# Optimization experiments

Measured on AMD Instinct MI355X. Metric: run time of the kernel, lower is better.

## Reference

```python
import jax, jax.numpy as jnp
import numpy as np

EMBED_DIM = 1024
NUM_HEADS = 16
HEAD_DIM = EMBED_DIM // NUM_HEADS
SCALE = HEAD_DIM ** -0.5
B, T = 4, 2048


def setup_inputs() -> dict:
    key = jax.random.key(0)
    ks = jax.random.split(key, 5)
    s = EMBED_DIM ** -0.5
    return {
        "x": jax.random.normal(ks[0], (B, T, EMBED_DIM), dtype=jnp.float32),
        "w_qkv": jax.random.normal(ks[1], (EMBED_DIM, 3 * EMBED_DIM), dtype=jnp.float32) * s,
        "b_qkv": jnp.zeros((3 * EMBED_DIM,), dtype=jnp.float32),
        "w_out": jax.random.normal(ks[2], (EMBED_DIM, EMBED_DIM), dtype=jnp.float32) * s,
        "b_out": jnp.zeros((EMBED_DIM,), dtype=jnp.float32),
    }


def reference(x, w_qkv, b_qkv, w_out, b_out):
    Bz, Tz, C = x.shape
    qkv = x @ w_qkv + b_qkv                              # (B,T,3C)
    qkv = qkv.reshape(Bz, Tz, 3, NUM_HEADS, HEAD_DIM)
    q, k, v = (qkv[:, :, i].transpose(0, 2, 1, 3) for i in range(3))  # (B,H,T,Dh)
    attn = jnp.einsum('bhqd,bhkd->bhqk', q, k) * SCALE   # (B,H,T,T)
    attn = jax.nn.softmax(attn, axis=-1)
    out = jnp.einsum('bhqk,bhkd->bhqd', attn, v)         # (B,H,T,Dh)
    out = out.transpose(0, 2, 1, 3).reshape(Bz, Tz, C)
    return out @ w_out + b_out
```

## Files before the change

kernel.cpp:

```cpp
#include <hip/hip_runtime.h>
#include <stdint.h>

#define EMB   1024
#define NH    16
#define DH    64
#define NB    4
#define NT    2048
#define BT    (NB*NT)
#define NQKV  (3*EMB)
#define CL2E  0.1803368801111204f

typedef short v4s __attribute__((ext_vector_type(4)));
typedef short v8s __attribute__((ext_vector_type(8)));
typedef float v4f __attribute__((ext_vector_type(4)));

__device__ __forceinline__ unsigned short f2bf(float f) {
  unsigned int u = __builtin_bit_cast(unsigned int, f);
  u += 0x7fffu + ((u >> 16) & 1u);
  return (unsigned short)(u >> 16);
}

__device__ __forceinline__ void gld16(const unsigned short* g, unsigned short* l) {
  __builtin_amdgcn_global_load_lds(
      (const __attribute__((address_space(1))) unsigned int*)g,
      (__attribute__((address_space(3))) unsigned int*)l, 16, 0, 0);
}

__device__ __forceinline__ v4s exppack(v4f s) {
  unsigned int u0 = __builtin_bit_cast(unsigned int, exp2f(s[0])) + 0x8000u;
  unsigned int u1 = __builtin_bit_cast(unsigned int, exp2f(s[1])) + 0x8000u;
  unsigned int u2 = __builtin_bit_cast(unsigned int, exp2f(s[2])) + 0x8000u;
  unsigned int u3 = __builtin_bit_cast(unsigned int, exp2f(s[3])) + 0x8000u;
  uint2 d;
  d.x = __builtin_amdgcn_perm(u1, u0, 0x07060302u);
  d.y = __builtin_amdgcn_perm(u3, u2, 0x07060302u);
  return __builtin_bit_cast(v4s, d);
}

__global__ __launch_bounds__(256) void cast_bf16_k(
    const float* __restrict__ in, unsigned short* __restrict__ out, int n8) {
  int i = blockIdx.x * 256 + threadIdx.x;
  if (i >= n8) return;
  const float4* p = (const float4*)in + (size_t)i * 2;
  float4 a = p[0], b = p[1];
  union { unsigned short s[8]; uint4 u; } o;
  o.s[0] = f2bf(a.x); o.s[1] = f2bf(a.y); o.s[2] = f2bf(a.z); o.s[3] = f2bf(a.w);
  o.s[4] = f2bf(b.x); o.s[5] = f2bf(b.y); o.s[6] = f2bf(b.z); o.s[7] = f2bf(b.w);
  ((uint4*)out)[i] = o.u;
}

__global__ __launch_bounds__(256) void transpose_cast_k(
    const float* __restrict__ in, unsigned short* __restrict__ out, int R, int C) {
  __shared__ float tile[32][33];
  int t = threadIdx.x, lr = t >> 5, lc = t & 31;
  int r0 = blockIdx.y * 32, c0 = blockIdx.x * 32;
#pragma unroll
  for (int i = 0; i < 32; i += 8)
    tile[lr + i][lc] = in[(size_t)(r0 + lr + i) * C + c0 + lc];
  __syncthreads();
#pragma unroll
  for (int i = 0; i < 32; i += 8)
    out[(size_t)(c0 + lr + i) * R + r0 + lc] = f2bf(tile[lc][lr + i]);
}

template <int MODE>
__global__ __launch_bounds__(256, 2) void gemm_bt(
    const unsigned short* __restrict__ A, const unsigned short* __restrict__ Bt,
    const float* __restrict__ bias, float* __restrict__ Co,
    unsigned short* __restrict__ q_out, unsigned short* __restrict__ k_out,
    unsigned short* __restrict__ v_out, int M, int N, int K) {
  const int t = threadIdx.x;
  const int wave = t >> 6, lane = t & 63;
  const int m16 = lane & 15, quad = lane >> 4;
  const int wr = wave >> 1, wc = wave & 1;
  const int bm = blockIdx.y * 128, bn = blockIdx.x * 128;

  __shared__ unsigned short As[128 * 32];
  __shared__ unsigned short Bs[128 * 32];

  v4f acc[4][4];
#pragma unroll
  for (int mi = 0; mi < 4; mi++)
#pragma unroll
    for (int ni = 0; ni < 4; ni++) acc[mi][ni] = (v4f){0.f, 0.f, 0.f, 0.f};

  const int sF = (m16 ^ (m16 >> 2)) & 3;

  const int cA = t, rA = cA >> 2, jA = (cA & 3) ^ ((rA ^ (rA >> 2)) & 3);
  const int cB = 256 + t, rB = cB >> 2, jB = (cB & 3) ^ ((rB ^ (rB >> 2)) & 3);
  const unsigned short* gA0 = A + (size_t)(bm + rA) * K + jA * 8;
  const unsigned short* gA1 = A + (size_t)(bm + rB) * K + jB * 8;
  const unsigned short* gB0 = Bt + (size_t)(bn + rA) * K + jA * 8;
  const unsigned short* gB1 = Bt + (size_t)(bn + rB) * K + jB * 8;
  const unsigned short* aBase = &As[(wr * 64 + m16) * 32 + ((quad ^ sF) * 8)];
  const unsigned short* bBase = &Bs[(wc * 64 + m16) * 32 + ((quad ^ sF) * 8)];

  const int nkt = K >> 5;
  for (int kt = 0; kt < nkt; ++kt) {
    gld16(gA0, &As[cA * 8]);
    gld16(gA1, &As[cB * 8]);
    gld16(gB0, &Bs[cA * 8]);
    gld16(gB1, &Bs[cB * 8]);
    gA0 += 32; gA1 += 32; gB0 += 32; gB1 += 32;
    __syncthreads();

    v8s a[4], b[4];
#pragma unroll
    for (int mi = 0; mi < 4; mi++)
      a[mi] = *(const v8s*)(aBase + mi * 16 * 32);
#pragma unroll
    for (int ni = 0; ni < 4; ni++)
      b[ni] = *(const v8s*)(bBase + ni * 16 * 32);
#pragma unroll
    for (int mi = 0; mi < 4; mi++)
#pragma unroll
      for (int ni = 0; ni < 4; ni++)
        acc[mi][ni] = __builtin_amdgcn_mfma_f32_16x16x32_bf16(a[mi], b[ni], acc[mi][ni], 0, 0, 0);
    __syncthreads();
  }

  if (MODE == 0) {
#pragma unroll
    for (int mi = 0; mi < 4; mi++) {
#pragma unroll
      for (int ni = 0; ni < 4; ni++) {
        int col = bn + wc * 64 + ni * 16 + m16;
        int which = col >> 10;
        int h = (col >> 6) & 15, d = col & 63;
        float bv = bias[col];
        float sc = (which == 0) ? CL2E : 1.f;
        int row0 = bm + wr * 64 + mi * 16 + quad * 4;
        int bb = row0 >> 11, tt0 = row0 & 2047;
        float v0 = (acc[mi][ni][0] + bv) * sc, v1 = (acc[mi][ni][1] + bv) * sc;
        float v2 = (acc[mi][ni][2] + bv) * sc, v3 = (acc[mi][ni][3] + bv) * sc;
        if (which == 2) {
          ushort4 pk; pk.x = f2bf(v0); pk.y = f2bf(v1); pk.z = f2bf(v2); pk.w = f2bf(v3);
          *(ushort4*)&v_out[(((size_t)(bb * NH + h)) * DH + d) * NT + tt0] = pk;
        } else {
          unsigned short* dst = (which == 0) ? q_out : k_out;
          size_t idx = (((size_t)(bb * NH + h)) * NT + tt0) * DH + d;
          dst[idx] = f2bf(v0); dst[idx + DH] = f2bf(v1);
          dst[idx + 2 * DH] = f2bf(v2); dst[idx + 3 * DH] = f2bf(v3);
        }
      }
    }
  } else {
#pragma unroll
    for (int mi = 0; mi < 4; mi++) {
#pragma unroll
      for (int ni = 0; ni < 4; ni++) {
        int col = bn + wc * 64 + ni * 16 + m16;
        float bv = bias[col];
#pragma unroll
        for (int r = 0; r < 4; r++) {
          int row = bm + wr * 64 + mi * 16 + quad * 4 + r;
          Co[(size_t)row * N + col] = acc[mi][ni][r] + bv;
        }
      }
    }
  }
}

__global__ __launch_bounds__(256, 3) void flash_attn(
    const unsigned short* __restrict__ Qg, const unsigned short* __restrict__ Kg,
    const unsigned short* __restrict__ Vtg, unsigned short* __restrict__ Og) {
  const int t = threadIdx.x;
  const int w = t >> 6, lane = t & 63;
  const int m16 = lane & 15, quad = lane >> 4;
  const int qt = blockIdx.x, bh = blockIdx.y;
  const int b = bh >> 4, h = bh & 15;

  __shared__ unsigned short Ks[128 * 64];
  __shared__ unsigned short Vt[64 * 128];

  const size_t baseq = (size_t)bh * NT * DH;
  const size_t basev = (size_t)bh * DH * NT;

  v8s qf[2][2];
#pragma unroll
  for (int tq = 0; tq < 2; tq++) {
    int qrow = qt * 128 + w * 32 + tq * 16 + m16;
#pragma unroll
    for (int kk = 0; kk < 2; kk++)
      qf[tq][kk] = *(const v8s*)&Qg[baseq + (size_t)qrow * DH + kk * 32 + quad * 8];
  }

  v4f accO[2][4], accL[2];
#pragma unroll
  for (int tq = 0; tq < 2; tq++) {
#pragma unroll
    for (int i = 0; i < 4; i++) accO[tq][i] = (v4f){0.f, 0.f, 0.f, 0.f};
    accL[tq] = (v4f){0.f, 0.f, 0.f, 0.f};
  }
  const v4f zero4 = (v4f){0.f, 0.f, 0.f, 0.f};
  const v4s ones4 = (v4s){(short)0x3F80, (short)0x3F80, (short)0x3F80, (short)0x3F80};

  const int sK = m16 & 7;
  const int rK = t >> 3, jK = (t & 7) ^ (rK & 7);
  const int dV = t >> 4, jV = (t & 15) ^ (dV & 15);
  const unsigned short* gK = &Kg[baseq + (size_t)rK * DH + jK * 8];
  const unsigned short* gV = &Vtg[basev + (size_t)dV * NT + jV * 8];
  const unsigned short* kb0 = &Ks[m16 * 64 + (((0 * 4 + quad) ^ sK) * 8)];
  const unsigned short* kb1 = &Ks[m16 * 64 + (((1 * 4 + quad) ^ sK) * 8)];
  const int qh = quad >> 1, q1 = quad & 1;
  const unsigned short* vBase = &Vt[m16 * 128 + q1 * 4];

  for (int kt = 0; kt < NT / 128; ++kt) {
    __syncthreads();
#pragma unroll
    for (int i = 0; i < 4; ++i)
      gld16(gK + (size_t)(i * 32) * DH, &Ks[(i * 256 + t) * 8]);
#pragma unroll
    for (int i = 0; i < 4; ++i)
      gld16(gV + (size_t)(i * 16) * NT, &Vt[(i * 256 + t) * 8]);
    gK += 128 * DH;
    gV += 128;
    __syncthreads();

    v4s pp[2][8];
#pragma unroll
    for (int ni = 0; ni < 8; ni++) {
      v8s k0 = *(const v8s*)(kb0 + ni * 1024);
      v8s k1 = *(const v8s*)(kb1 + ni * 1024);
      v4f s0 = __builtin_amdgcn_mfma_f32_16x16x32_bf16(k0, qf[0][0], zero4, 0, 0, 0);
      s0 = __builtin_amdgcn_mfma_f32_16x16x32_bf16(k1, qf[0][1], s0, 0, 0, 0);
      v4f s1 = __builtin_amdgcn_mfma_f32_16x16x32_bf16(k0, qf[1][0], zero4, 0, 0, 0);
      s1 = __builtin_amdgcn_mfma_f32_16x16x32_bf16(k1, qf[1][1], s1, 0, 0, 0);
      pp[0][ni] = exppack(s0);
      pp[1][ni] = exppack(s1);
    }

#pragma unroll
    for (int ni = 0; ni < 8; ni++) {
      accL[0] = __builtin_amdgcn_mfma_f32_16x16x16bf16_1k(ones4, pp[0][ni], accL[0], 0, 0, 0);
      accL[1] = __builtin_amdgcn_mfma_f32_16x16x16bf16_1k(ones4, pp[1][ni], accL[1], 0, 0, 0);
      const unsigned short* vA = vBase + (((ni * 2 + qh) ^ m16) * 8);
#pragma unroll
      for (int ni2 = 0; ni2 < 4; ni2++) {
        v4s vf = *(const v4s*)(vA + ni2 * 2048);
        accO[0][ni2] = __builtin_amdgcn_mfma_f32_16x16x16bf16_1k(vf, pp[0][ni], accO[0][ni2], 0, 0, 0);
        accO[1][ni2] = __builtin_amdgcn_mfma_f32_16x16x16bf16_1k(vf, pp[1][ni], accO[1][ni2], 0, 0, 0);
      }
    }
  }

#pragma unroll
  for (int tq = 0; tq < 2; tq++) {
    float inv = 1.f / accL[tq][0];
    int trow = qt * 128 + w * 32 + tq * 16 + m16;
    size_t ob = ((size_t)b * NT + trow) * EMB + h * DH;
#pragma unroll
    for (int ni2 = 0; ni2 < 4; ni2++) {
      float v0 = accO[tq][ni2][0] * inv, v1 = accO[tq][ni2][1] * inv;
      float v2 = accO[tq][ni2][2] * inv, v3 = accO[tq][ni2][3] * inv;
      uint2 d;
      d.x = (unsigned int)f2bf(v0) | ((unsigned int)f2bf(v1) << 16);
      d.y = (unsigned int)f2bf(v2) | ((unsigned int)f2bf(v3) << 16);
      *(uint2*)&Og[ob + ni2 * 16 + quad * 4] = d;
    }
  }
}

extern "C" void kernel_launch(void* const* d_in, const int* in_sizes, int n_in,
                              void* d_out, int out_size, void* d_ws, size_t ws_size,
                              hipStream_t stream) {
  const float* x     = (const float*)d_in[0];
  const float* w_qkv = (const float*)d_in[1];
  const float* b_qkv = (const float*)d_in[2];
  const float* w_out = (const float*)d_in[3];
  const float* b_out = (const float*)d_in[4];
  float* out = (float*)d_out;

  unsigned short* xb    = (unsigned short*)d_ws;
  unsigned short* wqkvT = xb    + (size_t)BT * EMB;
  unsigned short* woutT = wqkvT + (size_t)NQKV * EMB;
  unsigned short* qb    = woutT + (size_t)EMB * EMB;
  unsigned short* kb    = qb    + (size_t)NB * NH * NT * DH;
  unsigned short* vb    = kb    + (size_t)NB * NH * NT * DH;
  unsigned short* ao    = vb    + (size_t)NB * NH * NT * DH;

  cast_bf16_k<<<(BT * EMB / 8 + 255) / 256, 256, 0, stream>>>(x, xb, BT * EMB / 8);
  transpose_cast_k<<<dim3(NQKV / 32, EMB / 32), 256, 0, stream>>>(w_qkv, wqkvT, EMB, NQKV);
  transpose_cast_k<<<dim3(EMB / 32, EMB / 32), 256, 0, stream>>>(w_out, woutT, EMB, EMB);

  gemm_bt<0><<<dim3(NQKV / 128, BT / 128), 256, 0, stream>>>(
      xb, wqkvT, b_qkv, nullptr, qb, kb, vb, BT, NQKV, EMB);

  flash_attn<<<dim3(NT / 128, NB * NH), 256, 0, stream>>>(qb, kb, vb, ao);

  gemm_bt<1><<<dim3(EMB / 128, BT / 128), 256, 0, stream>>>(
      ao, woutT, b_out, out, nullptr, nullptr, nullptr, BT, EMB, EMB);
}
```

Before: 310.0 us.

## Use 16x16x32 bf16 MFMA for PV with remapped K layout and packed exp conversion

The PV and row-sum products switch from 16x16x16 MFMAs to 16x16x32 MFMAs, which halves the instruction count. To supply that, the K tile in LDS gets a new swizzle and key mapping so each lane's two QK^T results form the 8 contiguous keys the wider B operand needs. Exponentials now use the native exp2 builtin and the hardware v_cvt_pk_bf16_f32 instruction in place of manual rounding bit tricks. The risks are LDS bank conflicts from the new swizzle and a subtle key-order mismatch between the P fragments and the V reads.

```diff
diff --git a/kernel.cpp b/kernel.cpp
--- a/kernel.cpp
+++ b/kernel.cpp
@@ -26,15 +26,19 @@
       (__attribute__((address_space(3))) unsigned int*)l, 16, 0, 0);
 }
 
-__device__ __forceinline__ v4s exppack(v4f s) {
-  unsigned int u0 = __builtin_bit_cast(unsigned int, exp2f(s[0])) + 0x8000u;
-  unsigned int u1 = __builtin_bit_cast(unsigned int, exp2f(s[1])) + 0x8000u;
-  unsigned int u2 = __builtin_bit_cast(unsigned int, exp2f(s[2])) + 0x8000u;
-  unsigned int u3 = __builtin_bit_cast(unsigned int, exp2f(s[3])) + 0x8000u;
-  uint2 d;
-  d.x = __builtin_amdgcn_perm(u1, u0, 0x07060302u);
-  d.y = __builtin_amdgcn_perm(u3, u2, 0x07060302u);
-  return __builtin_bit_cast(v4s, d);
+__device__ __forceinline__ unsigned int cvtpk_bf16(float lo, float hi) {
+  unsigned int r;
+  asm("v_cvt_pk_bf16_f32 %0, %1, %2" : "=v"(r) : "v"(lo), "v"(hi));
+  return r;
+}
+
+__device__ __forceinline__ v8s exppack8(v4f a, v4f b) {
+  uint4 d;
+  d.x = cvtpk_bf16(__builtin_amdgcn_exp2f(a[0]), __builtin_amdgcn_exp2f(a[1]));
+  d.y = cvtpk_bf16(__builtin_amdgcn_exp2f(a[2]), __builtin_amdgcn_exp2f(a[3]));
+  d.z = cvtpk_bf16(__builtin_amdgcn_exp2f(b[0]), __builtin_amdgcn_exp2f(b[1]));
+  d.w = cvtpk_bf16(__builtin_amdgcn_exp2f(b[2]), __builtin_amdgcn_exp2f(b[3]));
+  return __builtin_bit_cast(v8s, d);
 }
 
 __global__ __launch_bounds__(256) void cast_bf16_k(
@@ -193,17 +197,20 @@
     accL[tq] = (v4f){0.f, 0.f, 0.f, 0.f};
   }
   const v4f zero4 = (v4f){0.f, 0.f, 0.f, 0.f};
-  const v4s ones4 = (v4s){(short)0x3F80, (short)0x3F80, (short)0x3F80, (short)0x3F80};
-
-  const int sK = m16 & 7;
-  const int rK = t >> 3, jK = (t & 7) ^ (rK & 7);
+  const v8s ones8 = (v8s){(short)0x3F80, (short)0x3F80, (short)0x3F80, (short)0x3F80,
+                          (short)0x3F80, (short)0x3F80, (short)0x3F80, (short)0x3F80};
+
+  const int rK = t >> 3, jK = (t & 7) ^ (((rK & 3) << 1) | ((rK >> 3) & 1));
   const int dV = t >> 4, jV = (t & 15) ^ (dV & 15);
   const unsigned short* gK = &Kg[baseq + (size_t)rK * DH + jK * 8];
   const unsigned short* gV = &Vtg[basev + (size_t)dV * NT + jV * 8];
-  const unsigned short* kb0 = &Ks[m16 * 64 + (((0 * 4 + quad) ^ sK) * 8)];
-  const unsigned short* kb1 = &Ks[m16 * 64 + (((1 * 4 + quad) ^ sK) * 8)];
-  const int qh = quad >> 1, q1 = quad & 1;
-  const unsigned short* vBase = &Vt[m16 * 128 + q1 * 4];
+  const int keyA = ((m16 >> 2) << 3) | (m16 & 3);
+  const int sP = ((m16 & 3) << 1) | ((m16 >> 2) & 1);
+  const unsigned short* ka0 = &Ks[ keyA      * 64 + ((0 + quad) ^ sP) * 8];
+  const unsigned short* ka1 = &Ks[ keyA      * 64 + ((4 + quad) ^ sP) * 8];
+  const unsigned short* kb0 = &Ks[(keyA + 4) * 64 + ((0 + quad) ^ sP) * 8];
+  const unsigned short* kb1 = &Ks[(keyA + 4) * 64 + ((4 + quad) ^ sP) * 8];
+  const unsigned short* vBase = &Vt[m16 * 128];
 
   for (int kt = 0; kt < NT / 128; ++kt) {
     __syncthreads();
@@ -217,29 +224,36 @@
     gV += 128;
     __syncthreads();
 
-    v4s pp[2][8];
-#pragma unroll
-    for (int ni = 0; ni < 8; ni++) {
-      v8s k0 = *(const v8s*)(kb0 + ni * 1024);
-      v8s k1 = *(const v8s*)(kb1 + ni * 1024);
-      v4f s0 = __builtin_amdgcn_mfma_f32_16x16x32_bf16(k0, qf[0][0], zero4, 0, 0, 0);
-      s0 = __builtin_amdgcn_mfma_f32_16x16x32_bf16(k1, qf[0][1], s0, 0, 0, 0);
-      v4f s1 = __builtin_amdgcn_mfma_f32_16x16x32_bf16(k0, qf[1][0], zero4, 0, 0, 0);
-      s1 = __builtin_amdgcn_mfma_f32_16x16x32_bf16(k1, qf[1][1], s1, 0, 0, 0);
-      pp[0][ni] = exppack(s0);
-      pp[1][ni] = exppack(s1);
-    }
-
-#pragma unroll
-    for (int ni = 0; ni < 8; ni++) {
-      accL[0] = __builtin_amdgcn_mfma_f32_16x16x16bf16_1k(ones4, pp[0][ni], accL[0], 0, 0, 0);
-      accL[1] = __builtin_amdgcn_mfma_f32_16x16x16bf16_1k(ones4, pp[1][ni], accL[1], 0, 0, 0);
-      const unsigned short* vA = vBase + (((ni * 2 + qh) ^ m16) * 8);
+    v8s pp[2][4];
+#pragma unroll
+    for (int nj = 0; nj < 4; nj++) {
+      const int o = nj * 2048;
+      v8s kA0 = *(const v8s*)(ka0 + o);
+      v8s kA1 = *(const v8s*)(ka1 + o);
+      v8s kB0 = *(const v8s*)(kb0 + o);
+      v8s kB1 = *(const v8s*)(kb1 + o);
+      v4f s0a = __builtin_amdgcn_mfma_f32_16x16x32_bf16(kA0, qf[0][0], zero4, 0, 0, 0);
+      s0a = __builtin_amdgcn_mfma_f32_16x16x32_bf16(kA1, qf[0][1], s0a, 0, 0, 0);
+      v4f s1a = __builtin_amdgcn_mfma_f32_16x16x32_bf16(kA0, qf[1][0], zero4, 0, 0, 0);
+      s1a = __builtin_amdgcn_mfma_f32_16x16x32_bf16(kA1, qf[1][1], s1a, 0, 0, 0);
+      v4f s0b = __builtin_amdgcn_mfma_f32_16x16x32_bf16(kB0, qf[0][0], zero4, 0, 0, 0);
+      s0b = __builtin_amdgcn_mfma_f32_16x16x32_bf16(kB1, qf[0][1], s0b, 0, 0, 0);
+      v4f s1b = __builtin_amdgcn_mfma_f32_16x16x32_bf16(kB0, qf[1][0], zero4, 0, 0, 0);
+      s1b = __builtin_amdgcn_mfma_f32_16x16x32_bf16(kB1, qf[1][1], s1b, 0, 0, 0);
+      pp[0][nj] = exppack8(s0a, s0b);
+      pp[1][nj] = exppack8(s1a, s1b);
+    }
+
+#pragma unroll
+    for (int nj = 0; nj < 4; nj++) {
+      accL[0] = __builtin_amdgcn_mfma_f32_16x16x32_bf16(ones8, pp[0][nj], accL[0], 0, 0, 0);
+      accL[1] = __builtin_amdgcn_mfma_f32_16x16x32_bf16(ones8, pp[1][nj], accL[1], 0, 0, 0);
+      const int slot = ((nj * 4 + quad) ^ m16) * 8;
 #pragma unroll
       for (int ni2 = 0; ni2 < 4; ni2++) {
-        v4s vf = *(const v4s*)(vA + ni2 * 2048);
-        accO[0][ni2] = __builtin_amdgcn_mfma_f32_16x16x16bf16_1k(vf, pp[0][ni], accO[0][ni2], 0, 0, 0);
-        accO[1][ni2] = __builtin_amdgcn_mfma_f32_16x16x16bf16_1k(vf, pp[1][ni], accO[1][ni2], 0, 0, 0);
+        v8s vf = *(const v8s*)(vBase + ni2 * 16 * 128 + slot);
+        accO[0][ni2] = __builtin_amdgcn_mfma_f32_16x16x32_bf16(vf, pp[0][nj], accO[0][ni2], 0, 0, 0);
+        accO[1][ni2] = __builtin_amdgcn_mfma_f32_16x16x32_bf16(vf, pp[1][nj], accO[1][ni2], 0, 0, 0);
       }
     }
   }
```

Result: faster. 280.6 us, median of 2 (-9.5%).
